# Kernel tuning notes

Measured on AMD Instinct MI355X. Metric: run time of the kernel, lower is better.

The kernel has to match this reference:

```python
import jax, jax.numpy as jnp
import numpy as np

T, B, E = 2048, 16, 1024   # time, batch, embed_dim (fairseq T x B x C layout)
CDIM = 1024                # conv_dim
H = 16                     # num_heads
K = 31                     # kernel_size, padding_l = K-1 (causal left pad)


def _xavier(k, shape):
    fan_out, fan_in = shape
    lim = float(np.sqrt(6.0 / (fan_in + fan_out)))
    return jax.random.uniform(k, shape, jnp.float32, -lim, lim)


def setup_inputs() -> dict:
    key = jax.random.key(0)
    ks = jax.random.split(key, 5)
    return {
        "x": jax.random.normal(ks[0], (T, B, E), jnp.float32),
        "w1": _xavier(ks[1], (CDIM, E)),
        "b1": jnp.zeros((CDIM,), jnp.float32),
        "ww": _xavier(ks[2], (H * K, CDIM)),  # DynamicConv weight_linear
        "bw": jnp.zeros((H * K,), jnp.float32),
        "w2": _xavier(ks[3], (E, CDIM)),
        "b2": jnp.zeros((E,), jnp.float32),
        "gamma": jnp.ones((E,), jnp.float32),
        "beta": jnp.zeros((E,), jnp.float32),
    }


def layer_norm(x, g, b, eps=1e-5):
    m = x.mean(-1, keepdims=True)
    v = ((x - m) ** 2).mean(-1, keepdims=True)
    return (x - m) * jax.lax.rsqrt(v + eps) * g + b


def dynamic_conv(h, ww, bw):
    # h: [T, B, C]; per-position softmax kernel weights shared across R=C/H channels per head
    Tn, Bn, C = h.shape
    R = C // H
    w = jax.nn.softmax((h @ ww.T + bw).reshape(Tn, Bn, H, K), axis=-1)  # [T,B,H,K]
    hp = jnp.pad(h.reshape(Tn, Bn, H, R), ((K - 1, 0), (0, 0), (0, 0), (0, 0)))
    # out[t] = sum_k w[t,:,:,k] * h[t + k - (K-1)]  (causal banded aggregation)
    acc = jnp.zeros((Tn, Bn, H, R), h.dtype)
    for k in range(K):  # fixed small kernel-size loop, not a data-dim loop
        acc = acc + w[:, :, :, k:k + 1] * hp[k:k + Tn]
    return acc.reshape(Tn, Bn, C)


def reference(x, w1, b1, ww, bw, w2, b2, gamma, beta):
    # eval mode: all dropouts are identity; normalize_before=False -> LN after residual
    h = x @ w1.T + b1            # linear1: [T,B,E] -> [T,B,CDIM]
    h = dynamic_conv(h, ww, bw)  # DynamicConv, weight_softmax=True, no conv bias
    h = h @ w2.T + b2            # linear2: back to embed_dim
    return layer_norm(x + h, gamma, beta)
```

## Files before the change

kernel.cpp:

```cpp
#include <hip/hip_runtime.h>

#define T_DIM 2048
#define B_DIM 16
#define E_DIM 1024
#define CD    1024
#define NH    16
#define KSZ   31
#define M_DIM 32768
#define SLICE 131072
#define BSTRIDE 2097152

typedef unsigned int u32;
typedef unsigned short u16;
typedef __attribute__((ext_vector_type(8))) __bf16 bf16x8;
typedef __attribute__((ext_vector_type(4))) float f32x4;
typedef __attribute__((ext_vector_type(4))) float fvec4;
typedef __attribute__((ext_vector_type(8))) unsigned short us8;
typedef __attribute__((ext_vector_type(4))) unsigned short us4;
typedef __attribute__((ext_vector_type(4))) unsigned int ui4;

__device__ __forceinline__ float bf2f(u16 u) {
  union { float f; u32 i; } c; c.i = ((u32)u) << 16; return c.f;
}
__device__ __forceinline__ u16 f2bf(float f) {
  union { float f; u32 i; } c; c.f = f;
  u32 u = c.i;
  u += 0x7fffu + ((u >> 16) & 1u);
  return (u16)(u >> 16);
}

#define GLDS(gp, lp)                                                        \
  __builtin_amdgcn_global_load_lds(                                         \
      (__attribute__((address_space(1))) void*)(gp),                        \
      (__attribute__((address_space(3))) void*)(lp), 16, 0, 0)

__global__ __launch_bounds__(256) void prep(const float* __restrict__ x,
                                            const float* __restrict__ w1,
                                            const float* __restrict__ w2,
                                            const float* __restrict__ ww,
                                            u16* __restrict__ xbt,
                                            u16* __restrict__ w1b,
                                            u16* __restrict__ w2b,
                                            u16* __restrict__ wwb,
                                            u16* __restrict__ zreg)
{
  const int NX = (T_DIM * B_DIM * E_DIM) / 4;
  const int N1 = NX + (CD * E_DIM) / 4;
  const int N2 = N1 + (E_DIM * CD) / 4;
  const int N3 = N2 + (NH * KSZ * CD) / 4;
  int i = blockIdx.x * 256 + threadIdx.x;
  if (i < NX) {
    int rr = i >> 8, c = i & 255;
    int t = rr >> 4, b = rr & 15;
    fvec4 v = ((const fvec4*)x)[i];
    us4 o;
    o[0] = f2bf(v[0]); o[1] = f2bf(v[1]); o[2] = f2bf(v[2]); o[3] = f2bf(v[3]);
    ((us4*)xbt)[(size_t)(b * T_DIM + t) * 256 + c] = o;
  } else if (i < N1) {
    int j = i - NX;
    fvec4 v = ((const fvec4*)w1)[j];
    us4 o;
    o[0] = f2bf(v[0]); o[1] = f2bf(v[1]); o[2] = f2bf(v[2]); o[3] = f2bf(v[3]);
    ((us4*)w1b)[j] = o;
  } else if (i < N2) {
    int j = i - N1;
    fvec4 v = ((const fvec4*)w2)[j];
    us4 o;
    o[0] = f2bf(v[0]); o[1] = f2bf(v[1]); o[2] = f2bf(v[2]); o[3] = f2bf(v[3]);
    ((us4*)w2b)[j] = o;
  } else if (i < N3) {
    int j = i - N2;
    fvec4 v = ((const fvec4*)ww)[j];
    us4 o;
    o[0] = f2bf(v[0]); o[1] = f2bf(v[1]); o[2] = f2bf(v[2]); o[3] = f2bf(v[3]);
    ((us4*)wwb)[j] = o;
  } else {
    ((ui4*)zreg)[i - N3] = (ui4)(0u);
  }
}

template<int OUT_MODE, int GUARD_N, int A_CONV>
__global__ __launch_bounds__(256, 2) void gemm_tlp(
    const u16* __restrict__ A, const u16* __restrict__ B,
    const float* __restrict__ bias, void* __restrict__ Cout,
    int N, int K, int ldc, int ntn)
{
  __shared__ u16 sA[2][128 * 32];
  __shared__ u16 sB[2][256 * 32];
  const int tid = threadIdx.x;
  const int lane = tid & 63;
  const int wid = tid >> 6;
  const int wc = wid;

  const int swz = (blockIdx.x & 7) * (gridDim.x >> 3) + (blockIdx.x >> 3);
  const int bm = (swz / ntn) * 128;
  const int bn = (swz % ntn) * 256;

  const int srow = tid >> 2;
  const int scol = (tid & 3) * 8;
  const int scols = scol ^ (((srow >> 1) & 3) << 3);
  const int sdst = srow * 32 + scol;

  const u16* gA2[2];
  #pragma unroll
  for (int it = 0; it < 2; it++) {
    int rr = bm + it * 64 + srow;
    if (A_CONV)
      gA2[it] = A + (size_t)(rr >> 11) * BSTRIDE + (size_t)(rr & 2047) * 64 + scols;
    else
      gA2[it] = A + (size_t)rr * K + scols;
  }
  const u16* gB2[4];
  #pragma unroll
  for (int it = 0; it < 4; it++) {
    int br = bn + it * 64 + srow;
    if (GUARD_N) br = min(br, N - 1);
    gB2[it] = B + (size_t)br * K + scols;
  }

  auto stage = [&](int ph) {
    int slot = ph & 1;
    int kt = ph >> 1, kh = ph & 1;
    size_t koA = A_CONV ? (size_t)kt * SLICE + kh * 32 : (size_t)kt * 64 + kh * 32;
    size_t koB = (size_t)kt * 64 + kh * 32;
    GLDS(gA2[0] + koA, &sA[slot][0 * 2048 + sdst]);
    GLDS(gA2[1] + koA, &sA[slot][1 * 2048 + sdst]);
    GLDS(gB2[0] + koB, &sB[slot][0 * 2048 + sdst]);
    GLDS(gB2[1] + koB, &sB[slot][1 * 2048 + sdst]);
    GLDS(gB2[2] + koB, &sB[slot][2 * 2048 + sdst]);
    GLDS(gB2[3] + koB, &sB[slot][3 * 2048 + sdst]);
  };

  f32x4 acc[8][4];
  #pragma unroll
  for (int i = 0; i < 8; i++)
    #pragma unroll
    for (int j = 0; j < 4; j++) acc[i][j] = (f32x4)(0.0f);

  const int fr = lane & 15;
  const int g8 = (lane >> 4) * 8;

  auto ard = [&](const u16* base, int row) -> bf16x8 {
    return *(const bf16x8*)&base[row * 32 + (g8 ^ ((((row >> 1) & 3)) << 3))];
  };

  const int NP = K >> 5;

  stage(0);
  asm volatile("s_waitcnt vmcnt(0)" ::: "memory");
  __builtin_amdgcn_s_barrier();

  for (int ph = 0; ph < NP; ph++) {
    const int cur = ph & 1;
    bf16x8 bF[4], aG[8];
    #pragma unroll
    for (int n = 0; n < 4; n++) bF[n] = ard(&sB[cur][0], wc * 64 + n * 16 + fr);
    #pragma unroll
    for (int mi = 0; mi < 8; mi++) aG[mi] = ard(&sA[cur][0], mi * 16 + fr);
    if (ph + 1 < NP) stage(ph + 1);
    asm volatile("s_waitcnt lgkmcnt(0)" ::: "memory");
    __builtin_amdgcn_sched_barrier(0);
    __builtin_amdgcn_s_setprio(1);
    #pragma unroll
    for (int mi = 0; mi < 8; mi++)
      #pragma unroll
      for (int n = 0; n < 4; n++)
        acc[mi][n] = __builtin_amdgcn_mfma_f32_16x16x32_bf16(aG[mi], bF[n], acc[mi][n], 0, 0, 0);
    __builtin_amdgcn_s_setprio(0);
    __builtin_amdgcn_sched_barrier(0);
    asm volatile("s_waitcnt vmcnt(0)" ::: "memory");
    __builtin_amdgcn_s_barrier();
  }

  const int orow0 = bm + (lane >> 4) * 4;
  const int ocol0 = bn + wc * 64 + fr;
  #pragma unroll
  for (int m = 0; m < 8; m++) {
    #pragma unroll
    for (int n = 0; n < 4; n++) {
      #pragma unroll
      for (int q = 0; q < 4; q++) {
        int row = orow0 + m * 16 + q;
        int col = ocol0 + n * 16;
        if (!GUARD_N || col < N) {
          float v = acc[m][n][q] + bias[col];
          if (OUT_MODE == 1) {
            ((u16*)Cout)[(size_t)row * ldc + col] = f2bf(v);
          } else if (OUT_MODE == 2) {
            int bb = row >> 11, t = row & 2047;
            int hh = col / 31, kk = col - hh * 31;
            ((u16*)Cout)[((size_t)((bb * NH + hh) * T_DIM + t)) * 32 + kk] = f2bf(v);
          } else {
            int bb = row >> 11, t = row & 2047;
            ((u16*)Cout)[(size_t)((bb << 4) + (col >> 6)) * SLICE + (size_t)t * 64 + (col & 63)] = f2bf(v);
          }
        }
      }
    }
  }
}

__global__ __launch_bounds__(256) void dconv(const u16* __restrict__ h1,
                                             const u16* __restrict__ wt,
                                             const u16* __restrict__ zreg,
                                             u16* __restrict__ outc)
{
  constexpr int TT = 128, HALO = 30, SW = 33;
  int bid = blockIdx.x;
  int tt = bid & 15;
  int b  = (bid >> 4) & 15;
  int h  = bid >> 8;
  int s  = b * 16 + h;
  int t0 = tt * TT;
  __shared__ u16 hl[(TT + HALO) * 64];
  __shared__ float wl[TT * SW];
  int tid = threadIdx.x;

  const u16* slice = h1 + (size_t)s * SLICE;
  #pragma unroll
  for (int it = 0; it < 5; it++) {
    int c = it * 256 + tid;
    if (c < (TT + HALO) * 8) {
      int row = t0 - HALO + (c >> 3);
      const u16* src = slice + (size_t)row * 64 + (c & 7) * 8;
      if (row < 0) src = zreg + (c & 7) * 8;
      GLDS(src, hl + c * 8);
    }
  }
  {
    const u16* wsrc = wt + ((size_t)s * T_DIM + t0) * 32;
    #pragma unroll
    for (int it = 0; it < 2; it++) {
      int j = (it * 256 + tid) * 8;
      us8 v = *(const us8*)(wsrc + j);
      int row = j >> 5, col = j & 31;
      #pragma unroll
      for (int e = 0; e < 8; e++) wl[row * SW + col + e] = bf2f(v[e]);
    }
  }
  __syncthreads();

  if (tid < TT) {
    float* p = wl + tid * SW;
    float v[KSZ];
    float mx = -1e30f;
    #pragma unroll
    for (int k = 0; k < KSZ; k++) { v[k] = p[k]; mx = fmaxf(mx, v[k]); }
    float sum = 0.f;
    #pragma unroll
    for (int k = 0; k < KSZ; k++) { v[k] = __expf(v[k] - mx); sum += v[k]; }
    float inv = 1.0f / sum;
    #pragma unroll
    for (int k = 0; k < KSZ; k++) p[k] = v[k] * inv;
  }
  __syncthreads();

  int rb = (tid & 7) * 8;
  int tl = tid >> 3;

  #pragma unroll
  for (int half = 0; half < 4; half++) {
    const int tb = tl + half * 32;
    const float* wp = wl + tb * SW;
    const u16* hb = hl + tb * 64 + rb;
    float acc[8];
    #pragma unroll
    for (int e = 0; e < 8; e++) acc[e] = 0.f;
    #pragma unroll
    for (int k = 0; k < KSZ; k++) {
      us8 hv = *(const us8*)(hb + k * 64);
      float w = wp[k];
      #pragma unroll
      for (int e = 0; e < 8; e++) acc[e] += w * bf2f(hv[e]);
    }
    us8 o;
    #pragma unroll
    for (int e = 0; e < 8; e++) o[e] = f2bf(acc[e]);
    *(us8*)(outc + (size_t)s * SLICE + (size_t)(t0 + tb) * 64 + rb) = o;
  }
}

__global__ __launch_bounds__(256) void ln_res(const u16* __restrict__ xb,
                                              const u16* __restrict__ hb,
                                              float* __restrict__ out,
                                              const float* __restrict__ gamma,
                                              const float* __restrict__ beta)
{
  int mp = blockIdx.x;
  int b = mp >> 11, t = mp & 2047;
  int xrow = t * 16 + b;
  const us4* xr = (const us4*)(xb + (size_t)mp * E_DIM);
  const us4* hr = (const us4*)(hb + (size_t)mp * E_DIM);
  fvec4* yr = (fvec4*)(out + (size_t)xrow * E_DIM);
  int tid = threadIdx.x;
  us4 hv = hr[tid];
  us4 xv = xr[tid];
  fvec4 s;
  #pragma unroll
  for (int e = 0; e < 4; e++) s[e] = bf2f(xv[e]) + bf2f(hv[e]);
  float sum = s[0] + s[1] + s[2] + s[3];
  float sq  = s[0]*s[0] + s[1]*s[1] + s[2]*s[2] + s[3]*s[3];
  #pragma unroll
  for (int off = 32; off >= 1; off >>= 1) {
    sum += __shfl_xor(sum, off, 64);
    sq  += __shfl_xor(sq, off, 64);
  }
  __shared__ float red[8];
  int lane = tid & 63, wid = tid >> 6;
  if (lane == 0) { red[wid] = sum; red[4 + wid] = sq; }
  __syncthreads();
  sum = red[0] + red[1] + red[2] + red[3];
  sq  = red[4] + red[5] + red[6] + red[7];
  float mean = sum * (1.0f / E_DIM);
  float var  = sq * (1.0f / E_DIM) - mean * mean;
  float rstd = rsqrtf(var + 1e-5f);
  fvec4 g = ((const fvec4*)gamma)[tid];
  fvec4 be = ((const fvec4*)beta)[tid];
  fvec4 o;
  #pragma unroll
  for (int e = 0; e < 4; e++) o[e] = (s[e] - mean) * rstd * g[e] + be[e];
  yr[tid] = o;
}

extern "C" void kernel_launch(void* const* d_in, const int* in_sizes, int n_in,
                              void* d_out, int out_size, void* d_ws, size_t ws_size,
                              hipStream_t stream)
{
  const float* x     = (const float*)d_in[0];
  const float* w1    = (const float*)d_in[1];
  const float* b1    = (const float*)d_in[2];
  const float* ww    = (const float*)d_in[3];
  const float* bw    = (const float*)d_in[4];
  const float* w2    = (const float*)d_in[5];
  const float* b2    = (const float*)d_in[6];
  const float* gamma = (const float*)d_in[7];
  const float* beta  = (const float*)d_in[8];
  float* out = (float*)d_out;

  char* ws = (char*)d_ws;
  u16*   xbt  = (u16*)(ws);
  u16*   h1p  = (u16*)(ws + ((size_t)64 << 20));
  u16*   wt   = (u16*)(ws + ((size_t)128 << 20));
  u16*   convp = (u16*)(ws + ((size_t)160 << 20));
  u16*   w1b  = (u16*)(ws + ((size_t)224 << 20));
  u16*   w2b  = (u16*)(ws + ((size_t)226 << 20));
  u16*   wwb  = (u16*)(ws + ((size_t)228 << 20));
  u16*   zreg = (u16*)(ws + ((size_t)230 << 20));
  u16*   h2p  = h1p;

  prep<<<35313, 256, 0, stream>>>(x, w1, w2, ww, xbt, w1b, w2b, wwb, zreg);

  gemm_tlp<3, 0, 0><<<1024, 256, 0, stream>>>(xbt, w1b, b1, h1p, CD, E_DIM, 0, 4);
  gemm_tlp<2, 1, 1><<<512, 256, 0, stream>>>(h1p, wwb, bw, wt, NH * KSZ, CD, 0, 2);
  dconv<<<4096, 256, 0, stream>>>(h1p, wt, zreg, convp);
  gemm_tlp<1, 0, 1><<<1024, 256, 0, stream>>>(convp, w2b, b2, h2p, E_DIM, CD, E_DIM, 4);
  ln_res<<<32768, 256, 0, stream>>>(xbt, h2p, out, gamma, beta);
}
```

Baseline: 350.4 us.

## Register-block dynamic conv over 4 consecutive timesteps to reuse halo loads

Each thread now computes 4 consecutive time steps instead of 4 strided ones. Each loaded h row from shared memory feeds up to 4 accumulators, cutting LDS reads from 124 to 34 per thread, and weight reads are vectorised as float4 with the row stride padded to 36. The output is staged through shared memory so the global stores stay coalesced. This costs more registers, an extra barrier and an LDS staging pass. The dconv kernel is only one part of the full pipeline.

```diff
diff --git a/kernel.cpp b/kernel.cpp
--- a/kernel.cpp
+++ b/kernel.cpp
@@ -205,7 +205,7 @@
                                              const u16* __restrict__ zreg,
                                              u16* __restrict__ outc)
 {
-  constexpr int TT = 128, HALO = 30, SW = 33;
+  constexpr int TT = 128, HALO = 30, SW = 36;
   int bid = blockIdx.x;
   int tt = bid & 15;
   int b  = (bid >> 4) & 15;
@@ -242,40 +242,72 @@
 
   if (tid < TT) {
     float* p = wl + tid * SW;
-    float v[KSZ];
+    f32x4 v4[8];
+    #pragma unroll
+    for (int c = 0; c < 8; c++) v4[c] = *(const f32x4*)(p + c * 4);
     float mx = -1e30f;
     #pragma unroll
-    for (int k = 0; k < KSZ; k++) { v[k] = p[k]; mx = fmaxf(mx, v[k]); }
+    for (int k = 0; k < KSZ; k++) mx = fmaxf(mx, v4[k >> 2][k & 3]);
     float sum = 0.f;
     #pragma unroll
-    for (int k = 0; k < KSZ; k++) { v[k] = __expf(v[k] - mx); sum += v[k]; }
+    for (int k = 0; k < KSZ; k++) {
+      float e = __expf(v4[k >> 2][k & 3] - mx);
+      v4[k >> 2][k & 3] = e;
+      sum += e;
+    }
     float inv = 1.0f / sum;
     #pragma unroll
-    for (int k = 0; k < KSZ; k++) p[k] = v[k] * inv;
-  }
-  __syncthreads();
-
-  int rb = (tid & 7) * 8;
-  int tl = tid >> 3;
+    for (int k = 0; k < KSZ; k++) v4[k >> 2][k & 3] *= inv;
+    #pragma unroll
+    for (int c = 0; c < 8; c++) *(f32x4*)(p + c * 4) = v4[c];
+  }
+  __syncthreads();
+
+  const int rb = (tid & 7) * 8;
+  const int tl = tid >> 3;
+  const int base = tl * 4;
+
+  float acc[4][8];
+  #pragma unroll
+  for (int dt = 0; dt < 4; dt++)
+    #pragma unroll
+    for (int e = 0; e < 8; e++) acc[dt][e] = 0.f;
+
+  f32x4 w4[4];
+  #pragma unroll
+  for (int j = 0; j < 34; j++) {
+    us8 hv = *(const us8*)(&hl[(base + j) * 64 + rb]);
+    float hf[8];
+    #pragma unroll
+    for (int e = 0; e < 8; e++) hf[e] = bf2f(hv[e]);
+    #pragma unroll
+    for (int dt = 0; dt < 4; dt++) {
+      const int k = j - dt;
+      if (k >= 0 && k <= 30) {
+        if ((k & 3) == 0)
+          w4[dt] = *(const f32x4*)(&wl[(base + dt) * SW + k]);
+        float w = w4[dt][k & 3];
+        #pragma unroll
+        for (int e = 0; e < 8; e++) acc[dt][e] += w * hf[e];
+      }
+    }
+  }
+
+  __syncthreads();
+  u16* ob = (u16*)wl;
+  #pragma unroll
+  for (int dt = 0; dt < 4; dt++) {
+    us8 o;
+    #pragma unroll
+    for (int e = 0; e < 8; e++) o[e] = f2bf(acc[dt][e]);
+    *(us8*)(&ob[(base + dt) * 64 + rb]) = o;
+  }
+  __syncthreads();
 
   #pragma unroll
   for (int half = 0; half < 4; half++) {
     const int tb = tl + half * 32;
-    const float* wp = wl + tb * SW;
-    const u16* hb = hl + tb * 64 + rb;
-    float acc[8];
-    #pragma unroll
-    for (int e = 0; e < 8; e++) acc[e] = 0.f;
-    #pragma unroll
-    for (int k = 0; k < KSZ; k++) {
-      us8 hv = *(const us8*)(hb + k * 64);
-      float w = wp[k];
-      #pragma unroll
-      for (int e = 0; e < 8; e++) acc[e] += w * bf2f(hv[e]);
-    }
-    us8 o;
-    #pragma unroll
-    for (int e = 0; e < 8; e++) o[e] = f2bf(acc[e]);
+    us8 o = *(const us8*)(&ob[tb * 64 + rb]);
     *(us8*)(outc + (size_t)s * SLICE + (size_t)(t0 + tb) * 64 + rb) = o;
   }
 }
```

New measurement: 360.0 us. 2.7% more time.
